# Kernel optimization log

Hardware: AMD Instinct MI355X
Metric: run time of the kernel (lower is better)

## Reference

```python
import jax, jax.numpy as jnp
import numpy as np

N = 10000            # nodes
E = 320000           # edges (avg degree 32)
L = 4                # layers
S = 64               # hidden 0e multiplicity
V = 16               # hidden 1o multiplicity
EMB = 32             # node-attr embedding dim
NB = 8               # bessel basis per channel (r and v -> 2*NB edge feats)
MR = 2.5             # max_radius
DEG = 32.0           # num_neighbors
GS = S + V           # gate input scalars: 64 scalars + 16 gates
NW = S * 2 + V * 2 + V * 2   # 192 per-edge tensor-product weights
MAXT = 100           # max atom types


def _semi_unitary(K):
    # Newton-Schulz orthogonalization: K^T K -> I (semi-unitary uplift matrix)
    K = K / jnp.linalg.norm(K)
    for _ in range(10):
        K = 1.5 * K - 0.5 * K @ (K.T @ K)
    return K


def _smooth_cutoff(t):
    u = 2.0 * (t - 1.0)
    y = (1.0 - jnp.cos(jnp.pi * u)) * 0.5
    return jnp.where(u > 0, 0.0, jnp.where(u < -1.0, 1.0, y))


def _edge_geom(d):
    # d: (E,3) edge vector. Returns cutoff-weighted 1x1o SH (component norm) and bessel features.
    r = jnp.linalg.norm(d, axis=1)                       # (E,)
    sh = np.sqrt(3.0) * d / r[:, None]                   # spherical harmonics 1x1o
    attr = _smooth_cutoff(r / MR)[:, None] * sh          # (E,3)
    k = jnp.arange(1, NB + 1, dtype=jnp.float32) * jnp.pi
    feat = np.sqrt(2.0 / MR) * jnp.sin(k * (r / MR)[:, None]) / r[:, None]
    return attr, feat * np.sqrt(NB)                      # (E,3), (E,NB)


def _fctp(s, v, attr, Ws, Wv):
    # FullyConnectedTensorProduct with pure-scalar (0e) node attr == attr-weighted per-irrep linear
    os = jnp.einsum('ni,ne,oie->no', s, attr, Ws) / np.sqrt(s.shape[1] * EMB)
    ov = jnp.einsum('nim,ne,oie->nom', v, attr, Wv) / np.sqrt(v.shape[1] * EMB)
    return os, ov


def _forward(x, node_attr, edge_src, edge_dst, emb_table, PU_K, h, mix,
             si_Ws, si_Wv, sc_Ws, sc_Wv, lin1_Ws, lin1_Wv, lin2_Ws, lin2_Wv,
             fc_W1, fc_b1, fc_W2, fc_b2, fc_W3, fc_b3):
    attr = emb_table[node_attr]                          # (N,EMB)
    K = _semi_unitary(PU_K)                              # (V,2)
    yv = jnp.einsum('ui,nim->num', K, x.reshape(N, 2, 3))  # uplift vectors
    ys = jnp.zeros((N, S), x.dtype)
    ys_old, yv_old = ys, yv
    c_s, c_x = np.sin(np.pi / 8), np.cos(np.pi / 8)
    for i in range(L):
        ar, fr = _edge_geom(x[:, :3][edge_src] - x[:, :3][edge_dst])
        av, fv = _edge_geom(x[:, 3:][edge_src] - x[:, 3:][edge_dst])
        a = jnp.stack([ar, av], axis=1)                  # (E,2,3) = 2x1o edge attr
        ef = jnp.concatenate([fr, fv], axis=1)           # (E,2*NB)
        # radial MLP -> per-edge TP weights
        hd = jax.nn.silu(ef @ fc_W1[i] + fc_b1[i])
        hd = jax.nn.silu(hd @ fc_W2[i] + fc_b2[i])
        w = hd @ fc_W3[i] + fc_b3[i]                     # (E,NW)
        w1 = w[:, :S * 2].reshape(-1, S, 2)
        w2 = w[:, S * 2:S * 2 + V * 2].reshape(-1, V, 2)
        w3 = w[:, S * 2 + V * 2:].reshape(-1, V, 2)
        # conv: lin1 -> gather -> TP -> scatter -> lin2 ; plus self-connection
        fs, fvv = _fctp(ys, yv, attr, lin1_Ws[i], lin1_Wv[i])
        s_src, v_src = fs[edge_src], fvv[edge_src]
        # 0e x 1o -> 1o (uvu)
        o1 = jnp.einsum('euv,eu,evm->eum', w1, s_src, a) / np.sqrt(2.0)   # (E,S,3)
        # 1o x 1o -> 0e (uvu)
        dots = jnp.einsum('eum,evm->euv', v_src, a)
        o2 = jnp.einsum('euv,euv->eu', w2, dots) / np.sqrt(6.0)           # (E,V)
        # 1o x 1o -> 1o (cross, uvu)
        cr = jnp.cross(v_src[:, :, None, :], a[:, None, :, :])            # (E,V,2,3)
        o3 = jnp.einsum('euv,euvm->eum', w3, cr) / 2.0                    # (E,V,3)
        mid_s = jax.ops.segment_sum(o2, edge_dst, num_segments=N) / np.sqrt(DEG)
        mid_v = jax.ops.segment_sum(jnp.concatenate([o1, o3], axis=1), edge_dst,
                                    num_segments=N) / np.sqrt(DEG)        # (N,S+V,3)
        cs2, cv2 = _fctp(mid_s, mid_v, attr, lin2_Ws[i], lin2_Wv[i])      # (N,GS),(N,V,3)
        scs, scv = _fctp(ys, yv, attr, sc_Ws[i], sc_Wv[i])
        conv_s = c_s * scs + c_x * cs2
        conv_v = c_s * scv + c_x * cv2
        # gate: silu scalars, sigmoid gates * gated vectors
        gns = jax.nn.silu(conv_s[:, :S])
        gnv = jax.nn.sigmoid(conv_s[:, S:])[:, :, None] * conv_v
        # self-interaction: per-irrep linear
        sis = ys @ si_Ws[i].T / np.sqrt(S)
        siv = jnp.einsum('oi,nim->nom', si_Wv[i], yv) / np.sqrt(V)
        # leapfrog update
        h2 = h[i] ** 2
        ns = 2.0 * ys - ys_old + h2 * (mix[i] * gns + (mix[i] - 1.0) * sis)
        nv = 2.0 * yv - yv_old + h2 * (mix[i] * gnv + (mix[i] - 1.0) * siv)
        ys_old, yv_old = ys, yv
        ys, yv = ns, nv
        x = jnp.einsum('ui,num->nim', K, yv).reshape(N, 6)   # project
    return x


def setup_inputs() -> dict:
    key = jax.random.key(0)
    ks = jax.random.split(key, 24)
    def g(i, sh, fan=1.0):
        return jax.random.normal(ks[i], sh, dtype=jnp.float32) / np.sqrt(fan)
    edge_src = jax.random.randint(ks[20], (E,), 0, N, dtype=jnp.int32)
    off = jax.random.randint(ks[21], (E,), 1, N, dtype=jnp.int32)
    edge_dst = (edge_src + off) % N                      # guarantees src != dst
    return {
        'x': g(0, (N, 6)),
        'batch': jnp.zeros((N,), jnp.int32),
        'node_attr': jax.random.randint(ks[22], (N,), 0, MAXT, dtype=jnp.int32),
        'edge_src': edge_src,
        'edge_dst': edge_dst,
        'emb_table': g(1, (MAXT, EMB)),
        'PU_K': g(2, (V, 2)),
        'h': jnp.full((L,), 0.01, jnp.float32),
        'mix': jnp.full((L,), 0.5, jnp.float32),
        'si_Ws': g(3, (L, S, S)), 'si_Wv': g(4, (L, V, V)),
        'sc_Ws': g(5, (L, GS, S, EMB)), 'sc_Wv': g(6, (L, V, V, EMB)),
        'lin1_Ws': g(7, (L, S, S, EMB)), 'lin1_Wv': g(8, (L, V, V, EMB)),
        'lin2_Ws': g(9, (L, GS, V, EMB)), 'lin2_Wv': g(10, (L, V, S + V, EMB)),
        'fc_W1': g(11, (L, 2 * NB, 64), 2 * NB), 'fc_b1': jnp.zeros((L, 64), jnp.float32),
        'fc_W2': g(12, (L, 64, 64), 64), 'fc_b2': jnp.zeros((L, 64), jnp.float32),
        'fc_W3': g(13, (L, 64, NW), 64), 'fc_b3': jnp.zeros((L, NW), jnp.float32),
    }


def reference(x, batch, node_attr, edge_src, edge_dst, emb_table, PU_K, h, mix,
              si_Ws, si_Wv, sc_Ws, sc_Wv, lin1_Ws, lin1_Wv, lin2_Ws, lin2_Wv,
              fc_W1, fc_b1, fc_W2, fc_b2, fc_W3, fc_b3):
    return _forward(x, node_attr, edge_src, edge_dst, emb_table, PU_K, h, mix,
                    si_Ws, si_Wv, sc_Ws, sc_Wv, lin1_Ws, lin1_Wv, lin2_Ws, lin2_Wv,
                    fc_W1, fc_b1, fc_W2, fc_b2, fc_W3, fc_b3)
```

## Files before the change

kernel.cpp:

```cpp
#include <hip/hip_runtime.h>
#include <hip/hip_fp8.h>
#include <math.h>

#define NN 10000
#define NE 320000
#define PI_F 3.14159265358979323846f

typedef __attribute__((ext_vector_type(8))) short short8x;
typedef __attribute__((ext_vector_type(4))) float float4x;

#if defined(__has_builtin)
#if __has_builtin(__builtin_amdgcn_cvt_pk_fp8_f32) && __has_builtin(__builtin_amdgcn_cvt_f32_fp8)
#define HW_FP8 1
#endif
#endif

__device__ __forceinline__ unsigned short f2b(float f) {
    unsigned b = __float_as_uint(f);
    return (unsigned short)((b + 0x7FFFu + ((b >> 16) & 1u)) >> 16);
}
__device__ __forceinline__ float silu(float x) {
    return x / (1.f + __expf(-x));
}
__device__ __forceinline__ unsigned char f2e4(float f) {
#ifdef HW_FP8
    int r = __builtin_amdgcn_cvt_pk_fp8_f32(f, f, 0, false);
    return (unsigned char)(r & 0xff);
#else
    __hip_fp8_e4m3 q(f);
    return (unsigned char)q.__x;
#endif
}
__device__ __forceinline__ float e42f(unsigned char v) {
#ifdef HW_FP8
    return __builtin_amdgcn_cvt_f32_fp8((int)v, 0);
#else
    __hip_fp8_e4m3 q;
    q.__x = (__hip_fp8_storage_t)v;
    return (float)q;
#endif
}
__device__ __forceinline__ float e4sel(unsigned word, int sel) {
#ifdef HW_FP8
    switch (sel & 3) {
        case 0:  return __builtin_amdgcn_cvt_f32_fp8((int)word, 0);
        case 1:  return __builtin_amdgcn_cvt_f32_fp8((int)word, 1);
        case 2:  return __builtin_amdgcn_cvt_f32_fp8((int)word, 2);
        default: return __builtin_amdgcn_cvt_f32_fp8((int)word, 3);
    }
#else
    return e42f((unsigned char)((word >> (8*(sel & 3))) & 0xffu));
#endif
}

__global__ void k_newton_kernel(const float* __restrict__ PU, float* __restrict__ Kout)
{
    if (threadIdx.x != 0 || blockIdx.x != 0) return;
    float K[32];
    float nrm = 0.f;
    for (int i = 0; i < 32; ++i) { K[i] = PU[i]; nrm += K[i]*K[i]; }
    float inv = 1.0f / sqrtf(nrm);
    for (int i = 0; i < 32; ++i) K[i] *= inv;
    for (int it = 0; it < 10; ++it) {
        float m00 = 0.f, m01 = 0.f, m11 = 0.f;
        for (int u = 0; u < 16; ++u) {
            float a = K[2*u], b = K[2*u+1];
            m00 += a*a; m01 += a*b; m11 += b*b;
        }
        for (int u = 0; u < 16; ++u) {
            float a = K[2*u], b = K[2*u+1];
            K[2*u]   = 1.5f*a - 0.5f*(a*m00 + b*m01);
            K[2*u+1] = 1.5f*b - 0.5f*(a*m01 + b*m11);
        }
    }
    for (int i = 0; i < 32; ++i) Kout[i] = K[i];
}

__global__ __launch_bounds__(256) void init_all_kernel(
    const float* __restrict__ x, const float* __restrict__ K,
    float* __restrict__ xp, float* __restrict__ yv0, float* __restrict__ yv1,
    float* __restrict__ ys0, float* __restrict__ ys1, float* __restrict__ fsb)
{
    int tid = blockIdx.x*256 + threadIdx.x;
    if (tid < NN*8) {
        int n = tid >> 3, c = tid & 7;
        xp[tid] = (c < 6) ? x[n*6 + c] : 0.f;
        return;
    }
    int t2 = tid - NN*8;
    if (t2 < NN*48) {
        int n = t2/48, j = t2%48, u = j/3, m = j%3;
        float v = K[2*u]*x[n*6+m] + K[2*u+1]*x[n*6+3+m];
        yv0[t2] = v; yv1[t2] = v;
        return;
    }
    t2 -= NN*48;
    if (t2 < NN*64) { ys0[t2] = 0.f; ys1[t2] = 0.f; fsb[t2] = 0.f; }
}

__global__ void init_fvv_kernel(const float* __restrict__ yv, const int* __restrict__ types,
                                const float* __restrict__ lin1vT0, float* __restrict__ fvv)
{
    int tid = blockIdx.x*blockDim.x + threadIdx.x;
    if (tid >= NN*48) return;
    int n = tid/48, j = tid%48, o = j/3, m = j%3;
    int t = types[n];
    const float* W = lin1vT0 + (size_t)t*256;
    float acc = 0.f;
    #pragma unroll
    for (int i = 0; i < 16; ++i) acc += yv[n*48 + i*3 + m]*W[i*16 + o];
    fvv[tid] = acc;
}

__device__ __forceinline__ void be_body(const float* __restrict__ W, const float* __restrict__ emb,
                                        float* __restrict__ out, int id, int O, int I, float scale)
{
    int o = id % O; int r = id / O;
    int i = r % I; r /= I;
    int t = r % 100; int l = r / 100;
    const float* w  = W + (((size_t)l*O + o)*I + i)*32;
    const float* em = emb + (size_t)t*32;
    float acc = 0.f;
    #pragma unroll
    for (int e = 0; e < 32; ++e) acc += w[e]*em[e];
    out[id] = acc*scale;
}

#define PREP_TOTAL (2048000 + 1638400 + 512000 + 512000 + 102400 + 102400 + 49152 + 16384 + 16384 + 8192 + 1024)
__global__ __launch_bounds__(256) void prep_kernel(
    const float* __restrict__ lin1_Ws, const float* __restrict__ lin1_Wv,
    const float* __restrict__ sc_Ws,   const float* __restrict__ sc_Wv,
    const float* __restrict__ lin2_Ws, const float* __restrict__ lin2_Wv,
    const float* __restrict__ si_Ws,   const float* __restrict__ si_Wv,
    const float* __restrict__ fc_W1,   const float* __restrict__ fc_W2,
    const float* __restrict__ fc_W3,   const float* __restrict__ emb,
    float* __restrict__ lin1sT, float* __restrict__ lin1vT,
    float* __restrict__ scsT,   float* __restrict__ scvT,
    float* __restrict__ lin2sT, float* __restrict__ lin2vT,
    float* __restrict__ siWsT,  float* __restrict__ siWvT,
    unsigned short* __restrict__ w1bp, unsigned short* __restrict__ w2bp,
    unsigned short* __restrict__ w3bf)
{
    const float s2048 = 0.022097086912079608f;
    const float s512  = 0.044194173824159216f;
    const float s2560 = 0.019764235376052372f;
    int tid = blockIdx.x*256 + threadIdx.x;
    if (tid < 2048000) { be_body(sc_Ws,   emb, scsT,   tid, 80, 64, s2048); return; }
    tid -= 2048000;
    if (tid < 1638400) { be_body(lin1_Ws, emb, lin1sT, tid, 64, 64, s2048); return; }
    tid -= 1638400;
    if (tid < 512000)  { be_body(lin2_Ws, emb, lin2sT, tid, 80, 16, s512);  return; }
    tid -= 512000;
    if (tid < 512000)  { be_body(lin2_Wv, emb, lin2vT, tid, 16, 80, s2560); return; }
    tid -= 512000;
    if (tid < 102400)  { be_body(lin1_Wv, emb, lin1vT, tid, 16, 16, s512);  return; }
    tid -= 102400;
    if (tid < 102400)  { be_body(sc_Wv,   emb, scvT,   tid, 16, 16, s512);  return; }
    tid -= 102400;
    if (tid < 49152) {
        int o = tid % 64; int r = tid / 64; int i = r % 192; int l = r / 192;
        w3bf[tid] = f2b(fc_W3[((size_t)l*64 + o)*192 + i]);
        return;
    }
    tid -= 49152;
    if (tid < 16384) {
        int o = tid % 64; int r = tid / 64; int i = r % 64; int l = r / 64;
        siWsT[tid] = si_Ws[((size_t)l*64 + o)*64 + i]*0.125f;
        return;
    }
    tid -= 16384;
    if (tid < 16384) {
        int kk = tid % 64; int r = tid / 64; int n = r % 64; int l = r / 64;
        w2bp[tid] = f2b(fc_W2[((size_t)l*64 + kk)*64 + n]);
        return;
    }
    tid -= 16384;
    if (tid < 8192) {
        int kk = tid % 32; int r = tid / 32; int n = r % 64; int l = r / 64;
        float v = (kk < 16) ? fc_W1[((size_t)l*16 + kk)*64 + n] : 0.f;
        w1bp[tid] = f2b(v);
        return;
    }
    tid -= 8192;
    if (tid < 1024) {
        int o = tid % 16; int r = tid / 16; int i = r % 16; int l = r / 16;
        siWvT[tid] = si_Wv[((size_t)l*16 + o)*16 + i]*0.25f;
    }
}

__global__ void hist_kernel(const int* __restrict__ dst, int* __restrict__ deg)
{
    int e = blockIdx.x*256 + threadIdx.x;
    if (e < NE) atomicAdd(&deg[dst[e]], 1);
}

__global__ __launch_bounds__(256) void scan_kernel(const int* __restrict__ deg,
                                                   int* __restrict__ segoff,
                                                   int* __restrict__ cursor)
{
    __shared__ int part[256];
    int tid = threadIdx.x;
    int base = tid*40;
    int s = 0;
    for (int i = 0; i < 40; ++i) { int idx = base+i; if (idx < NN) s += deg[idx]; }
    part[tid] = s;
    __syncthreads();
    for (int o = 1; o < 256; o <<= 1) {
        int v = (tid >= o) ? part[tid-o] : 0;
        __syncthreads();
        part[tid] += v;
        __syncthreads();
    }
    int excl = part[tid] - s;
    for (int i = 0; i < 40; ++i) {
        int idx = base+i;
        if (idx < NN) { segoff[idx] = excl; cursor[idx] = excl; excl += deg[idx]; }
        else if (idx == NN) { segoff[NN] = excl; }
    }
}

__global__ void scatter_kernel(const int* __restrict__ src, const int* __restrict__ dst,
                               int* __restrict__ cursor,
                               int* __restrict__ srcs, int* __restrict__ dsts)
{
    int e = blockIdx.x*256 + threadIdx.x;
    if (e >= NE) return;
    int d = dst[e];
    int p = atomicAdd(&cursor[d], 1);
    srcs[p] = src[e]; dsts[p] = d;
}

__global__ __launch_bounds__(256, 8) void edge_fused_kernel(
    const float* __restrict__ xp,
    const int* __restrict__ srcs, const int* __restrict__ dsts,
    const unsigned short* __restrict__ w1b,
    const float* __restrict__ b1,
    const unsigned short* __restrict__ w2b,
    const float* __restrict__ b2,
    const unsigned short* __restrict__ w3b,
    const float* __restrict__ b3,
    const float* __restrict__ fs, const float* __restrict__ fvv,
    float* __restrict__ mid)
{
    __shared__ __align__(16) unsigned char smem[64*196];
    __shared__ float abuf[64*6];
    __shared__ int ssrc[64], sdst[64];
    unsigned short* hbuf = (unsigned short*)smem;
    unsigned char*  wbuf = smem;
    int lane = threadIdx.x & 63;
    int wid  = threadIdx.x >> 6;
    int eblk = blockIdx.x * 64;
    int row16 = lane & 15, quad = lane >> 4;
    int erow = 16*wid + row16;

    if (threadIdx.x < 64) {
        ssrc[threadIdx.x] = srcs[eblk + threadIdx.x];
        sdst[threadIdx.x] = dsts[eblk + threadIdx.x];
    }

    if (lane < 32) {
        int eidx = 16*wid + (lane & 15);
        int half = lane >> 4;
        int p = eblk + eidx;
        int s = srcs[p], d = dsts[p];
        int off = 3*half;
        const float* xs = xp + (size_t)s*8 + off;
        const float* xd = xp + (size_t)d*8 + off;
        float d0 = xs[0]-xd[0], d1 = xs[1]-xd[1], d2 = xs[2]-xd[2];
        float r = sqrtf(d0*d0 + d1*d1 + d2*d2);
        float invr = 1.0f/r;
        float u = 0.8f*r - 2.0f;
        float cut = (u > 0.f) ? 0.f : ((u < -1.f) ? 1.f : 0.5f*(1.f - __cosf(PI_F*u)));
        float sc = 1.7320508075688772f*cut*invr;
        float* ab = abuf + eidx*6 + off;
        ab[0] = sc*d0; ab[1] = sc*d1; ab[2] = sc*d2;
        float fsc = 2.5298221281347035f*invr;
        float wr = 1.2566370614359172f*r;
        unsigned epk[4];
        #pragma unroll
        for (int k = 0; k < 4; ++k) {
            float e0 = fsc*__sinf((float)(2*k+1)*wr);
            float e1 = fsc*__sinf((float)(2*k+2)*wr);
            epk[k] = (unsigned)f2b(e0) | ((unsigned)f2b(e1) << 16);
        }
        uint4* hr = (uint4*)(hbuf + eidx*72);
        uint4 q; q.x = epk[0]; q.y = epk[1]; q.z = epk[2]; q.w = epk[3];
        hr[half] = q;
        uint4 qz; qz.x = 0; qz.y = 0; qz.z = 0; qz.w = 0;
        hr[2+half] = qz;
    }

    {
        short8x a = *(const short8x*)(hbuf + erow*72 + quad*8);
        float4x c[4];
        #pragma unroll
        for (int nt = 0; nt < 4; ++nt) {
            short8x b = *(const short8x*)(w1b + ((size_t)(nt*16 + row16))*32 + quad*8);
            c[nt] = __builtin_amdgcn_mfma_f32_16x16x32_bf16(a, b, (float4x){0.f,0.f,0.f,0.f}, 0, 0, 0);
        }
        #pragma unroll
        for (int nt = 0; nt < 4; ++nt) {
            float bias = b1[nt*16 + row16];
            #pragma unroll
            for (int r = 0; r < 4; ++r) {
                float h = silu(c[nt][r] + bias);
                hbuf[(16*wid + quad*4 + r)*72 + nt*16 + row16] = f2b(h);
            }
        }
    }
    {
        short8x a0v = *(const short8x*)(hbuf + erow*72 + 0*32 + quad*8);
        short8x a1v = *(const short8x*)(hbuf + erow*72 + 1*32 + quad*8);
        float4x c[4];
        #pragma unroll
        for (int nt = 0; nt < 4; ++nt) {
            short8x b0 = *(const short8x*)(w2b + ((size_t)(nt*16 + row16))*64 + 0*32 + quad*8);
            float4x t = __builtin_amdgcn_mfma_f32_16x16x32_bf16(a0v, b0, (float4x){0.f,0.f,0.f,0.f}, 0, 0, 0);
            short8x b1v = *(const short8x*)(w2b + ((size_t)(nt*16 + row16))*64 + 1*32 + quad*8);
            c[nt] = __builtin_amdgcn_mfma_f32_16x16x32_bf16(a1v, b1v, t, 0, 0, 0);
        }
        #pragma unroll
        for (int nt = 0; nt < 4; ++nt) {
            float bias = b2[nt*16 + row16];
            #pragma unroll
            for (int r = 0; r < 4; ++r) {
                float h = silu(c[nt][r] + bias);
                hbuf[(16*wid + quad*4 + r)*72 + nt*16 + row16] = f2b(h);
            }
        }
    }
    {
        short8x a0v = *(const short8x*)(hbuf + erow*72 + 0*32 + quad*8);
        short8x a1v = *(const short8x*)(hbuf + erow*72 + 1*32 + quad*8);
        __syncthreads();
        float4x acc[12];
        #pragma unroll
        for (int nt = 0; nt < 12; ++nt) {
            short8x b0 = *(const short8x*)(w3b + ((size_t)(nt*16 + row16))*64 + 0*32 + quad*8);
            float4x t = __builtin_amdgcn_mfma_f32_16x16x32_bf16(a0v, b0, (float4x){0.f,0.f,0.f,0.f}, 0, 0, 0);
            short8x b1v = *(const short8x*)(w3b + ((size_t)(nt*16 + row16))*64 + 1*32 + quad*8);
            acc[nt] = __builtin_amdgcn_mfma_f32_16x16x32_bf16(a1v, b1v, t, 0, 0, 0);
        }
        #pragma unroll
        for (int nt = 0; nt < 12; ++nt) {
            #pragma unroll
            for (int r = 0; r < 4; ++r) {
                wbuf[(16*wid + quad*4 + r)*196 + nt*16 + row16] = f2e4(acc[nt][r]);
            }
        }
    }
    __syncthreads();

    {
        int c = threadIdx.x;
        float acc = 0.f;
        int dprev = sdst[0];
        if (c < 192) {
            int u = c / 3;
            int m = c - 3*u;
            float bA = b3[2*u], bB = b3[2*u+1];
            const unsigned char* wp = wbuf + 2*u;
            const float* ap = abuf + m;
            const float* fsu = fs + u;
            #pragma unroll 4
            for (int e = 0; e < 64; ++e) {
                int d = sdst[e];
                if (d != dprev) {
                    atomicAdd(&mid[(size_t)dprev*256 + c], acc);
                    acc = 0.f; dprev = d;
                }
                int s = ssrc[e];
                float fsv = fsu[(size_t)s*64];
                unsigned w = *(const unsigned short*)(wp + e*196);
                float wa = e4sel(w, 0) + bA;
                float wb = e4sel(w, 1) + bB;
                float a0m = ap[e*6], a1m = ap[e*6 + 3];
                acc += fsv*0.125f*(wa*a0m + wb*a1m);
            }
            atomicAdd(&mid[(size_t)dprev*256 + c], acc);
        } else if (c < 208) {
            int u = c - 192;
            float bA = b3[128 + 2*u], bB = b3[129 + 2*u];
            const unsigned char* wp = wbuf + 128 + 2*u;
            const float* fvu = fvv + 3*u;
            #pragma unroll 2
            for (int e = 0; e < 64; ++e) {
                int d = sdst[e];
                if (d != dprev) {
                    atomicAdd(&mid[(size_t)dprev*256 + c], acc);
                    acc = 0.f; dprev = d;
                }
                int s = ssrc[e];
                const float* fv = fvu + (size_t)s*48;
                float v0 = fv[0], v1 = fv[1], v2 = fv[2];
                unsigned w = *(const unsigned short*)(wp + e*196);
                float w2a = e4sel(w, 0) + bA;
                float w2b = e4sel(w, 1) + bB;
                const float* ab = abuf + e*6;
                float dd0 = v0*ab[0] + v1*ab[1] + v2*ab[2];
                float dd1 = v0*ab[3] + v1*ab[4] + v2*ab[5];
                acc += (w2a*dd0 + w2b*dd1)*0.07216878364870323f;
            }
            atomicAdd(&mid[(size_t)dprev*256 + c], acc);
        } else {
            int j = c - 208;
            int u = j / 3;
            int m = j - 3*u;
            int m1 = (m == 2) ? 0 : (m + 1);
            int m2 = 3 - m - m1;
            float bA = b3[160 + 2*u], bB = b3[161 + 2*u];
            const unsigned char* wp = wbuf + 160 + 2*u;
            const float* fva = fvv + 3*u + m1;
            const float* fvb = fvv + 3*u + m2;
            #pragma unroll 2
            for (int e = 0; e < 64; ++e) {
                int d = sdst[e];
                if (d != dprev) {
                    atomicAdd(&mid[(size_t)dprev*256 + c], acc);
                    acc = 0.f; dprev = d;
                }
                int s = ssrc[e];
                float va = fva[(size_t)s*48];
                float vb = fvb[(size_t)s*48];
                unsigned w = *(const unsigned short*)(wp + e*196);
                float w3a = e4sel(w, 0) + bA;
                float w3b = e4sel(w, 1) + bB;
                const float* ab = abuf + e*6;
                float cx0 = va*ab[m2] - vb*ab[m1];
                float cx1 = va*ab[3 + m2] - vb*ab[3 + m1];
                acc += 0.08838834764831845f*(w3a*cx0 + w3b*cx1);
            }
            atomicAdd(&mid[(size_t)dprev*256 + c], acc);
        }
    }
}

__global__ __launch_bounds__(256) void node_update_kernel(
    const float* __restrict__ ys, const float* __restrict__ yv,
    float* __restrict__ ys_old, float* __restrict__ yv_old,
    const float* __restrict__ mid,
    const int* __restrict__ types,
    const float* __restrict__ scsT, const float* __restrict__ scvT,
    const float* __restrict__ lin2sT, const float* __restrict__ lin2vT,
    const float* __restrict__ siWsT, const float* __restrict__ siWvT,
    const float* __restrict__ lin1sTn, const float* __restrict__ lin1vTn,
    const float* __restrict__ Kbuf,
    const float* __restrict__ hv, const float* __restrict__ mixv, int layer,
    float* __restrict__ fs_out, float* __restrict__ fvv_out,
    float* __restrict__ xpad, float* __restrict__ dout)
{
    int n = blockIdx.x;
    int lane = threadIdx.x;
    __shared__ float ys_l[64], yv_l[48], mids[16], midv[240];
    __shared__ float conv_s[80], conv_v[48], sis_l[64], siv_l[48], ysn[64], yvn[48];
    int t = types[n];
    {
        float v = mid[(size_t)n*256 + lane];
        if (lane < 192) midv[lane] = v;
        else if (lane < 208) mids[lane-192] = v;
        else midv[192 + (lane-208)] = v;
    }
    if (lane < 64) ys_l[lane] = ys[n*64 + lane];
    else if (lane < 112) yv_l[lane-64] = yv[n*48 + (lane-64)];
    __syncthreads();
    if (lane < 80) {
        const float* Wsc = scsT + (size_t)t*5120;
        const float* W2s = lin2sT + (size_t)t*1280;
        float a_sc = 0.f, a_2 = 0.f;
        #pragma unroll
        for (int i = 0; i < 64; ++i) a_sc += ys_l[i]*Wsc[i*80 + lane];
        #pragma unroll
        for (int i = 0; i < 16; ++i) a_2 += mids[i]*W2s[i*80 + lane];
        conv_s[lane] = 0.3826834323650898f*a_sc + 0.9238795325112867f*a_2;
    } else if (lane < 144) {
        int o = lane - 80;
        float a_si = 0.f;
        #pragma unroll
        for (int i = 0; i < 64; ++i) a_si += ys_l[i]*siWsT[i*64 + o];
        sis_l[o] = a_si;
    } else if (lane < 192) {
        int j = lane - 144, o = j/3, m = j%3;
        const float* Wsc = scvT + (size_t)t*256;
        const float* W2v = lin2vT + (size_t)t*1280;
        float a_sc = 0.f, a_2 = 0.f, a_si = 0.f;
        #pragma unroll
        for (int i = 0; i < 16; ++i) {
            float y = yv_l[i*3+m];
            a_sc += y*Wsc[i*16+o];
            a_si += y*siWvT[i*16+o];
        }
        #pragma unroll
        for (int i = 0; i < 80; ++i) a_2 += midv[i*3+m]*W2v[i*16+o];
        conv_v[j] = 0.3826834323650898f*a_sc + 0.9238795325112867f*a_2;
        siv_l[j] = a_si;
    }
    __syncthreads();
    float hh = hv[layer]; float h2c = hh*hh; float mx = mixv[layer];
    if (lane < 64) {
        float cs = conv_s[lane];
        float gns = cs/(1.f + __expf(-cs));
        float ns = 2.f*ys_l[lane] - ys_old[n*64+lane] + h2c*(mx*gns + (mx-1.f)*sis_l[lane]);
        ys_old[n*64+lane] = ns;
        ysn[lane] = ns;
    } else if (lane < 112) {
        int j = lane-64, o = j/3;
        float g = 1.f/(1.f + __expf(-conv_s[64+o]));
        float gnv = g*conv_v[j];
        float nv = 2.f*yv_l[j] - yv_old[n*48+j] + h2c*(mx*gnv + (mx-1.f)*siv_l[j]);
        yv_old[n*48+j] = nv;
        yvn[j] = nv;
    }
    __syncthreads();
    if (lane < 6) {
        int i = lane/3, m = lane%3;
        float acc = 0.f;
        #pragma unroll
        for (int u = 0; u < 16; ++u) acc += Kbuf[2*u+i]*yvn[u*3+m];
        xpad[n*8 + lane] = acc;
        if (dout) dout[n*6 + lane] = acc;
    }
    if (lane < 64) {
        const float* W = lin1sTn + (size_t)t*4096;
        float acc = 0.f;
        #pragma unroll
        for (int i = 0; i < 64; ++i) acc += ysn[i]*W[i*64 + lane];
        fs_out[n*64 + lane] = acc;
    } else if (lane < 112) {
        int j = lane - 64, o = j/3, m = j%3;
        const float* W = lin1vTn + (size_t)t*256;
        float acc = 0.f;
        #pragma unroll
        for (int i = 0; i < 16; ++i) acc += yvn[i*3+m]*W[i*16 + o];
        fvv_out[n*48 + j] = acc;
    }
}

extern "C" void kernel_launch(void* const* d_in, const int* in_sizes, int n_in,
                              void* d_out, int out_size, void* d_ws, size_t ws_size,
                              hipStream_t stream)
{
    const float* x_in   = (const float*)d_in[0];
    const int*   types  = (const int*)  d_in[2];
    const int*   esrc   = (const int*)  d_in[3];
    const int*   edst   = (const int*)  d_in[4];
    const float* emb    = (const float*)d_in[5];
    const float* PU     = (const float*)d_in[6];
    const float* hv     = (const float*)d_in[7];
    const float* mixv   = (const float*)d_in[8];
    const float* si_Ws  = (const float*)d_in[9];
    const float* si_Wv  = (const float*)d_in[10];
    const float* sc_Ws  = (const float*)d_in[11];
    const float* sc_Wv  = (const float*)d_in[12];
    const float* lin1_Ws= (const float*)d_in[13];
    const float* lin1_Wv= (const float*)d_in[14];
    const float* lin2_Ws= (const float*)d_in[15];
    const float* lin2_Wv= (const float*)d_in[16];
    const float* fc_W1  = (const float*)d_in[17];
    const float* fc_b1  = (const float*)d_in[18];
    const float* fc_W2  = (const float*)d_in[19];
    const float* fc_b2  = (const float*)d_in[20];
    const float* fc_W3  = (const float*)d_in[21];
    const float* fc_b3  = (const float*)d_in[22];

    float* ws = (float*)d_ws;
    size_t off = 0;
    auto alloc = [&](size_t nf) { float* p = ws + off; off += nf; return p; };
    float* Kbuf   = alloc(64);
    float* x_pad  = alloc(80000);
    float* ys0    = alloc(640000);
    float* ys1    = alloc(640000);
    float* yv0    = alloc(480000);
    float* yv1    = alloc(480000);
    float* fsb    = alloc(640000);
    float* fvvb   = alloc(480000);
    float* midb   = alloc((size_t)NN*256);
    float* lin1sT = alloc((size_t)4*100*4096);
    float* lin1vT = alloc((size_t)4*100*256);
    float* scsT   = alloc((size_t)4*100*5120);
    float* scvT   = alloc((size_t)4*100*256);
    float* lin2sT = alloc((size_t)4*100*1280);
    float* lin2vT = alloc((size_t)4*100*1280);
    float* siWsT  = alloc((size_t)4*4096);
    float* siWvT  = alloc((size_t)4*256);
    int* iws = (int*)(ws + off);
    size_t ioff = 0;
    auto ialloc = [&](size_t ni) { int* p = iws + ioff; ioff += ni; return p; };
    int* deg    = ialloc(NN);
    int* segoff = ialloc(NN + 8);
    int* cursor = ialloc(NN);
    int* srcs   = ialloc(NE);
    int* dsts   = ialloc(NE);
    unsigned short* w1bp = (unsigned short*)(iws + ioff);
    unsigned short* w2bp = w1bp + (size_t)4*64*32;
    unsigned short* w3bf = w2bp + (size_t)4*64*64;

    k_newton_kernel<<<1, 1, 0, stream>>>(PU, Kbuf);
    prep_kernel<<<(PREP_TOTAL + 255)/256, 256, 0, stream>>>(
        lin1_Ws, lin1_Wv, sc_Ws, sc_Wv, lin2_Ws, lin2_Wv, si_Ws, si_Wv,
        fc_W1, fc_W2, fc_W3, emb,
        lin1sT, lin1vT, scsT, scvT, lin2sT, lin2vT, siWsT, siWvT,
        w1bp, w2bp, w3bf);
    {
        int tot = NN*8 + NN*48 + NN*64;
        init_all_kernel<<<(tot + 255)/256, 256, 0, stream>>>(
            x_in, Kbuf, x_pad, yv0, yv1, ys0, ys1, fsb);
    }
    init_fvv_kernel<<<(NN*48 + 255)/256, 256, 0, stream>>>(yv0, types, lin1vT, fvvb);

    (void)hipMemsetAsync(deg, 0, NN*sizeof(int), stream);
    hist_kernel<<<(NE+255)/256, 256, 0, stream>>>(edst, deg);
    scan_kernel<<<1, 256, 0, stream>>>(deg, segoff, cursor);
    scatter_kernel<<<(NE+255)/256, 256, 0, stream>>>(esrc, edst, cursor, srcs, dsts);

    float* ys_cur = ys0; float* ys_old = ys1;
    float* yv_cur = yv0; float* yv_old = yv1;
    for (int l = 0; l < 4; ++l) {
        (void)hipMemsetAsync(midb, 0, (size_t)NN*256*sizeof(float), stream);
        edge_fused_kernel<<<NE/64, 256, 0, stream>>>(
            x_pad, srcs, dsts,
            w1bp + (size_t)l*64*32,  fc_b1 + (size_t)l*64,
            w2bp + (size_t)l*64*64,  fc_b2 + (size_t)l*64,
            w3bf + (size_t)l*192*64, fc_b3 + (size_t)l*192,
            fsb, fvvb, midb);
        int ln = (l + 1) & 3;
        node_update_kernel<<<NN, 256, 0, stream>>>(
            ys_cur, yv_cur, ys_old, yv_old,
            midb, types,
            scsT   + (size_t)l*100*5120, scvT   + (size_t)l*100*256,
            lin2sT + (size_t)l*100*1280, lin2vT + (size_t)l*100*1280,
            siWsT  + (size_t)l*4096,     siWvT  + (size_t)l*256,
            lin1sT + (size_t)ln*100*4096, lin1vT + (size_t)ln*100*256,
            Kbuf, hv, mixv, l, fsb, fvvb,
            x_pad, (l == 3) ? (float*)d_out : nullptr);
        float* tmp;
        tmp = ys_cur; ys_cur = ys_old; ys_old = tmp;
        tmp = yv_cur; yv_cur = yv_old; yv_old = tmp;
    }
}
```

Before: 1.140 ms.

## Stage gathered source features in LDS transposed, vectorize edge reduction loop

The edge kernel now gathers each edge's source scalar and vector features into shared memory once, stored as bf16, pre-scaled and in a channel-major transposed layout. The per-edge weights and geometry buffers are also transposed so the reduction loop can read 4 edges at a time with vector LDS loads. Destination-change boundaries are precomputed as a ballot bitmask, so the atomic flush branch is only taken in chunks that contain a boundary. This removes repeated scattered global loads of fs/fvv per channel per edge, at the cost of more LDS (occupancy hint lowered from 8 to 5), extra bf16 rounding of features, and packed fp8 stores.

Result: faster. 936.2 us (-17.9%).

```diff
diff --git a/kernel.cpp b/kernel.cpp
--- a/kernel.cpp
+++ b/kernel.cpp
@@ -8,6 +8,7 @@
 
 typedef __attribute__((ext_vector_type(8))) short short8x;
 typedef __attribute__((ext_vector_type(4))) float float4x;
+typedef __attribute__((ext_vector_type(4))) unsigned short ushort4x;
 
 #if defined(__has_builtin)
 #if __has_builtin(__builtin_amdgcn_cvt_pk_fp8_f32) && __has_builtin(__builtin_amdgcn_cvt_f32_fp8)
@@ -18,6 +19,9 @@
 __device__ __forceinline__ unsigned short f2b(float f) {
     unsigned b = __float_as_uint(f);
     return (unsigned short)((b + 0x7FFFu + ((b >> 16) & 1u)) >> 16);
+}
+__device__ __forceinline__ float b2f(unsigned short u) {
+    return __uint_as_float(((unsigned)u) << 16);
 }
 __device__ __forceinline__ float silu(float x) {
     return x / (1.f + __expf(-x));
@@ -50,6 +54,16 @@
     }
 #else
     return e42f((unsigned char)((word >> (8*(sel & 3))) & 0xffu));
+#endif
+}
+__device__ __forceinline__ unsigned pk4(float a, float b, float c, float d) {
+#ifdef HW_FP8
+    unsigned w = (unsigned)__builtin_amdgcn_cvt_pk_fp8_f32(a, b, 0, false);
+    w = (unsigned)__builtin_amdgcn_cvt_pk_fp8_f32(c, d, (int)w, true);
+    return w;
+#else
+    return (unsigned)f2e4(a) | ((unsigned)f2e4(b) << 8) |
+           ((unsigned)f2e4(c) << 16) | ((unsigned)f2e4(d) << 24);
 #endif
 }
 
@@ -230,7 +244,7 @@
     srcs[p] = src[e]; dsts[p] = d;
 }
 
-__global__ __launch_bounds__(256, 8) void edge_fused_kernel(
+__global__ __launch_bounds__(256, 5) void edge_fused_kernel(
     const float* __restrict__ xp,
     const int* __restrict__ srcs, const int* __restrict__ dsts,
     const unsigned short* __restrict__ w1b,
@@ -242,11 +256,14 @@
     const float* __restrict__ fs, const float* __restrict__ fvv,
     float* __restrict__ mid)
 {
-    __shared__ __align__(16) unsigned char smem[64*196];
-    __shared__ float abuf[64*6];
-    __shared__ int ssrc[64], sdst[64];
+    __shared__ __align__(16) unsigned char smem[192*68];
+    __shared__ unsigned short fsl[64][68];
+    __shared__ unsigned short fvl[48][68];
+    __shared__ float abuf[6][68];
+    __shared__ int sdst[64];
+    __shared__ unsigned smaskl[2];
     unsigned short* hbuf = (unsigned short*)smem;
-    unsigned char*  wbuf = smem;
+    const float C3f = 0.08838834764831845f;
     int lane = threadIdx.x & 63;
     int wid  = threadIdx.x >> 6;
     int eblk = blockIdx.x * 64;
@@ -254,8 +271,14 @@
     int erow = 16*wid + row16;
 
     if (threadIdx.x < 64) {
-        ssrc[threadIdx.x] = srcs[eblk + threadIdx.x];
-        sdst[threadIdx.x] = dsts[eblk + threadIdx.x];
+        int tid = threadIdx.x;
+        int own = dsts[eblk + tid];
+        int pidx = eblk + tid - ((tid > 0) ? 1 : 0);
+        int prev = dsts[pidx];
+        sdst[tid] = own;
+        bool nb = (tid > 0) && (own != prev);
+        unsigned long long bm = __ballot(nb);
+        if (tid == 0) { smaskl[0] = (unsigned)bm; smaskl[1] = (unsigned)(bm >> 32); }
     }
 
     if (lane < 32) {
@@ -272,8 +295,9 @@
         float u = 0.8f*r - 2.0f;
         float cut = (u > 0.f) ? 0.f : ((u < -1.f) ? 1.f : 0.5f*(1.f - __cosf(PI_F*u)));
         float sc = 1.7320508075688772f*cut*invr;
-        float* ab = abuf + eidx*6 + off;
-        ab[0] = sc*d0; ab[1] = sc*d1; ab[2] = sc*d2;
+        abuf[off+0][eidx] = sc*d0;
+        abuf[off+1][eidx] = sc*d1;
+        abuf[off+2][eidx] = sc*d2;
         float fsc = 2.5298221281347035f*invr;
         float wr = 1.2566370614359172f*r;
         unsigned epk[4];
@@ -288,6 +312,30 @@
         hr[half] = q;
         uint4 qz; qz.x = 0; qz.y = 0; qz.z = 0; qz.w = 0;
         hr[2+half] = qz;
+    } else {
+        int eidx = 16*wid + (lane & 15);
+        int half = (lane >> 4) & 1;
+        int s = srcs[eblk + eidx];
+        const float4* fp = (const float4*)(fs + (size_t)s*64 + half*32);
+        #pragma unroll
+        for (int g = 0; g < 8; ++g) {
+            float4 t = fp[g];
+            int u0 = half*32 + g*4;
+            fsl[u0+0][eidx] = f2b(t.x*0.125f);
+            fsl[u0+1][eidx] = f2b(t.y*0.125f);
+            fsl[u0+2][eidx] = f2b(t.z*0.125f);
+            fsl[u0+3][eidx] = f2b(t.w*0.125f);
+        }
+        const float4* vp = (const float4*)(fvv + (size_t)s*48 + half*24);
+        #pragma unroll
+        for (int g = 0; g < 6; ++g) {
+            float4 t = vp[g];
+            int j0 = half*24 + g*4;
+            fvl[j0+0][eidx] = f2b(t.x*C3f);
+            fvl[j0+1][eidx] = f2b(t.y*C3f);
+            fvl[j0+2][eidx] = f2b(t.z*C3f);
+            fvl[j0+3][eidx] = f2b(t.w*C3f);
+        }
     }
 
     {
@@ -343,94 +391,144 @@
         }
         #pragma unroll
         for (int nt = 0; nt < 12; ++nt) {
-            #pragma unroll
-            for (int r = 0; r < 4; ++r) {
-                wbuf[(16*wid + quad*4 + r)*196 + nt*16 + row16] = f2e4(acc[nt][r]);
-            }
+            unsigned pw = pk4(acc[nt][0], acc[nt][1], acc[nt][2], acc[nt][3]);
+            *(unsigned*)(smem + (size_t)(nt*16 + row16)*68 + 16*wid + quad*4) = pw;
         }
     }
     __syncthreads();
 
     {
         int c = threadIdx.x;
+        unsigned mk0 = __builtin_amdgcn_readfirstlane(smaskl[0]);
+        unsigned mk1 = __builtin_amdgcn_readfirstlane(smaskl[1]);
         float acc = 0.f;
-        int dprev = sdst[0];
+        int dcur = sdst[0];
         if (c < 192) {
             int u = c / 3;
             int m = c - 3*u;
+            const unsigned char* wra = smem + (size_t)(2*u)*68;
+            const unsigned char* wrb = wra + 68;
+            const unsigned short* fsr = &fsl[u][0];
+            const float* a0r = &abuf[m][0];
+            const float* a1r = &abuf[3+m][0];
             float bA = b3[2*u], bB = b3[2*u+1];
-            const unsigned char* wp = wbuf + 2*u;
-            const float* ap = abuf + m;
-            const float* fsu = fs + u;
-            #pragma unroll 4
-            for (int e = 0; e < 64; ++e) {
-                int d = sdst[e];
-                if (d != dprev) {
-                    atomicAdd(&mid[(size_t)dprev*256 + c], acc);
-                    acc = 0.f; dprev = d;
+            for (int e4 = 0; e4 < 64; e4 += 4) {
+                unsigned wa4 = *(const unsigned*)(wra + e4);
+                unsigned wb4 = *(const unsigned*)(wrb + e4);
+                ushort4x f4v = *(const ushort4x*)(fsr + e4);
+                float4x a04 = *(const float4x*)(a0r + e4);
+                float4x a14 = *(const float4x*)(a1r + e4);
+                float q0 = b2f(f4v[0])*((e4sel(wa4,0)+bA)*a04[0] + (e4sel(wb4,0)+bB)*a14[0]);
+                float q1 = b2f(f4v[1])*((e4sel(wa4,1)+bA)*a04[1] + (e4sel(wb4,1)+bB)*a14[1]);
+                float q2 = b2f(f4v[2])*((e4sel(wa4,2)+bA)*a04[2] + (e4sel(wb4,2)+bB)*a14[2]);
+                float q3 = b2f(f4v[3])*((e4sel(wa4,3)+bA)*a04[3] + (e4sel(wb4,3)+bB)*a14[3]);
+                unsigned mch = ((e4 < 32) ? (mk0 >> e4) : (mk1 >> (e4-32))) & 15u;
+                if (mch == 0) {
+                    acc += (q0 + q1) + (q2 + q3);
+                } else {
+                    float q[4] = {q0, q1, q2, q3};
+                    #pragma unroll
+                    for (int k = 0; k < 4; ++k) {
+                        if (mch & (1u<<k)) {
+                            atomicAdd(&mid[(size_t)dcur*256 + c], acc);
+                            acc = 0.f; dcur = sdst[e4+k];
+                        }
+                        acc += q[k];
+                    }
                 }
-                int s = ssrc[e];
-                float fsv = fsu[(size_t)s*64];
-                unsigned w = *(const unsigned short*)(wp + e*196);
-                float wa = e4sel(w, 0) + bA;
-                float wb = e4sel(w, 1) + bB;
-                float a0m = ap[e*6], a1m = ap[e*6 + 3];
-                acc += fsv*0.125f*(wa*a0m + wb*a1m);
             }
-            atomicAdd(&mid[(size_t)dprev*256 + c], acc);
+            atomicAdd(&mid[(size_t)dcur*256 + c], acc);
         } else if (c < 208) {
             int u = c - 192;
+            const unsigned char* wra = smem + (size_t)(128 + 2*u)*68;
+            const unsigned char* wrb = wra + 68;
+            const unsigned short* v0r = &fvl[3*u+0][0];
+            const unsigned short* v1r = &fvl[3*u+1][0];
+            const unsigned short* v2r = &fvl[3*u+2][0];
             float bA = b3[128 + 2*u], bB = b3[129 + 2*u];
-            const unsigned char* wp = wbuf + 128 + 2*u;
-            const float* fvu = fvv + 3*u;
-            #pragma unroll 2
-            for (int e = 0; e < 64; ++e) {
-                int d = sdst[e];
-                if (d != dprev) {
-                    atomicAdd(&mid[(size_t)dprev*256 + c], acc);
-                    acc = 0.f; dprev = d;
+            const float FS = 0.8164965809277259f;
+            for (int e4 = 0; e4 < 64; e4 += 4) {
+                unsigned wa4 = *(const unsigned*)(wra + e4);
+                unsigned wb4 = *(const unsigned*)(wrb + e4);
+                ushort4x v04 = *(const ushort4x*)(v0r + e4);
+                ushort4x v14 = *(const ushort4x*)(v1r + e4);
+                ushort4x v24 = *(const ushort4x*)(v2r + e4);
+                float4x a00 = *(const float4x*)(&abuf[0][e4]);
+                float4x a01 = *(const float4x*)(&abuf[1][e4]);
+                float4x a02 = *(const float4x*)(&abuf[2][e4]);
+                float4x a10 = *(const float4x*)(&abuf[3][e4]);
+                float4x a11 = *(const float4x*)(&abuf[4][e4]);
+                float4x a12 = *(const float4x*)(&abuf[5][e4]);
+                float q[4];
+                #pragma unroll
+                for (int k = 0; k < 4; ++k) {
+                    float v0 = b2f(v04[k]), v1 = b2f(v14[k]), v2 = b2f(v24[k]);
+                    float dd0 = v0*a00[k] + v1*a01[k] + v2*a02[k];
+                    float dd1 = v0*a10[k] + v1*a11[k] + v2*a12[k];
+                    q[k] = (e4sel(wa4,k)+bA)*dd0 + (e4sel(wb4,k)+bB)*dd1;
                 }
-                int s = ssrc[e];
-                const float* fv = fvu + (size_t)s*48;
-                float v0 = fv[0], v1 = fv[1], v2 = fv[2];
-                unsigned w = *(const unsigned short*)(wp + e*196);
-                float w2a = e4sel(w, 0) + bA;
-                float w2b = e4sel(w, 1) + bB;
-                const float* ab = abuf + e*6;
-                float dd0 = v0*ab[0] + v1*ab[1] + v2*ab[2];
-                float dd1 = v0*ab[3] + v1*ab[4] + v2*ab[5];
-                acc += (w2a*dd0 + w2b*dd1)*0.07216878364870323f;
+                unsigned mch = ((e4 < 32) ? (mk0 >> e4) : (mk1 >> (e4-32))) & 15u;
+                if (mch == 0) {
+                    acc += (q[0] + q[1]) + (q[2] + q[3]);
+                } else {
+                    #pragma unroll
+                    for (int k = 0; k < 4; ++k) {
+                        if (mch & (1u<<k)) {
+                            atomicAdd(&mid[(size_t)dcur*256 + c], acc*FS);
+                            acc = 0.f; dcur = sdst[e4+k];
+                        }
+                        acc += q[k];
+                    }
+                }
             }
-            atomicAdd(&mid[(size_t)dprev*256 + c], acc);
+            atomicAdd(&mid[(size_t)dcur*256 + c], acc*FS);
         } else {
             int j = c - 208;
             int u = j / 3;
             int m = j - 3*u;
             int m1 = (m == 2) ? 0 : (m + 1);
             int m2 = 3 - m - m1;
+            const unsigned char* wra = smem + (size_t)(160 + 2*u)*68;
+            const unsigned char* wrb = wra + 68;
+            const unsigned short* var = &fvl[3*u+m1][0];
+            const unsigned short* vbr = &fvl[3*u+m2][0];
+            const float* am1a = &abuf[m1][0];
+            const float* am2a = &abuf[m2][0];
+            const float* am1b = &abuf[3+m1][0];
+            const float* am2b = &abuf[3+m2][0];
             float bA = b3[160 + 2*u], bB = b3[161 + 2*u];
-            const unsigned char* wp = wbuf + 160 + 2*u;
-            const float* fva = fvv + 3*u + m1;
-            const float* fvb = fvv + 3*u + m2;
-            #pragma unroll 2
-            for (int e = 0; e < 64; ++e) {
-                int d = sdst[e];
-                if (d != dprev) {
-                    atomicAdd(&mid[(size_t)dprev*256 + c], acc);
-                    acc = 0.f; dprev = d;
+            for (int e4 = 0; e4 < 64; e4 += 4) {
+                unsigned wa4 = *(const unsigned*)(wra + e4);
+                unsigned wb4 = *(const unsigned*)(wrb + e4);
+                ushort4x va4 = *(const ushort4x*)(var + e4);
+                ushort4x vb4 = *(const ushort4x*)(vbr + e4);
+                float4x a1m1 = *(const float4x*)(am1a + e4);
+                float4x a1m2 = *(const float4x*)(am2a + e4);
+                float4x a2m1 = *(const float4x*)(am1b + e4);
+                float4x a2m2 = *(const float4x*)(am2b + e4);
+                float q[4];
+                #pragma unroll
+                for (int k = 0; k < 4; ++k) {
+                    float va = b2f(va4[k]), vb = b2f(vb4[k]);
+                    float cx0 = va*a1m2[k] - vb*a1m1[k];
+                    float cx1 = va*a2m2[k] - vb*a2m1[k];
+                    q[k] = (e4sel(wa4,k)+bA)*cx0 + (e4sel(wb4,k)+bB)*cx1;
                 }
-                int s = ssrc[e];
-                float va = fva[(size_t)s*48];
-                float vb = fvb[(size_t)s*48];
-                unsigned w = *(const unsigned short*)(wp + e*196);
-                float w3a = e4sel(w, 0) + bA;
-                float w3b = e4sel(w, 1) + bB;
-                const float* ab = abuf + e*6;
-                float cx0 = va*ab[m2] - vb*ab[m1];
-                float cx1 = va*ab[3 + m2] - vb*ab[3 + m1];
-                acc += 0.08838834764831845f*(w3a*cx0 + w3b*cx1);
+                unsigned mch = ((e4 < 32) ? (mk0 >> e4) : (mk1 >> (e4-32))) & 15u;
+                if (mch == 0) {
+                    acc += (q[0] + q[1]) + (q[2] + q[3]);
+                } else {
+                    #pragma unroll
+                    for (int k = 0; k < 4; ++k) {
+                        if (mch & (1u<<k)) {
+                            atomicAdd(&mid[(size_t)dcur*256 + c], acc);
+                            acc = 0.f; dcur = sdst[e4+k];
+                        }
+                        acc += q[k];
+                    }
+                }
             }
-            atomicAdd(&mid[(size_t)dprev*256 + c], acc);
+            atomicAdd(&mid[(size_t)dcur*256 + c], acc);
         }
     }
 }
```
